# Optimization experiments

Hardware: AMD Instinct MI355X
Metric: run time of the kernel (lower is better)

The kernel has to match this reference:

```python
import jax, jax.numpy as jnp
import numpy as np


def make_hadamard(n, seed=1):
    # Sylvester Hadamard matrix with random sign diagonal, orthonormalized.
    assert (n & (n - 1)) == 0, 'n must be a power of 2'
    H = np.array([[1.0]], dtype=np.float32)
    while H.shape[0] < n:
        H = np.block([[H, H], [H, -H]])
    rng = np.random.default_rng(seed)
    signs = rng.choice(np.array([-1.0, 1.0], dtype=np.float32), size=n)
    H = (H * signs[None, :]) / np.sqrt(n, dtype=np.float32)
    return jnp.asarray(H)


def setup_inputs() -> dict:
    key = jax.random.key(0)
    k_x, = jax.random.split(key, 1)
    B, S, D = 4, 4096, 2048
    x = jax.random.normal(k_x, (B, S, D), dtype=jnp.float32)
    scale = jnp.ones((1,), dtype=jnp.float32) * 0.1  # must be > 0
    hadamard = make_hadamard(D)
    return {
        'x': x,
        'scale': scale,
        'hadamard': hadamard,
        'Qn': 8,
        'Qp': 7,
        'num_elements': B * S * D,
    }


def reference(x, scale, hadamard, Qn, Qp, num_elements):
    # grad_scale_mode == 'LSQ_grad_scale'
    qn = float(Qn)
    qp = float(Qp)
    grad_scale = 1.0 / jnp.sqrt(jnp.float32(num_elements) * qp)
    # scale = (scale - scale*gs).detach() + scale*gs  (forward value unchanged)
    bw_scale = scale * grad_scale
    s = jax.lax.stop_gradient(scale - bw_scale) + bw_scale  # shape [1]

    x_rot = jnp.matmul(x, hadamard)           # [B,S,D]
    xq = jnp.clip(x_rot / s, -qn, qp)
    # straight-through rounding: (round(x)-x).detach() + x
    yq = jax.lax.stop_gradient(jnp.round(xq) - xq) + xq
    y = yq * s
    return jnp.matmul(y, hadamard.T)          # un-rotate
```

## Files before the change

### kernel.cpp

```cpp
#include <hip/hip_runtime.h>
#include <math.h>


constexpr int D  = 2048;
constexpr int NR = 8;

__device__ __forceinline__ void fwht2048(float4 (&v)[NR], int lane) {
    #pragma unroll
    for (int r = 0; r < NR; ++r) {
        float a, b;
        a = v[r].x; b = v[r].y; v[r].x = a + b; v[r].y = a - b;
        a = v[r].z; b = v[r].w; v[r].z = a + b; v[r].w = a - b;
        a = v[r].x; b = v[r].z; v[r].x = a + b; v[r].z = a - b;
        a = v[r].y; b = v[r].w; v[r].y = a + b; v[r].w = a - b;
    }
    #pragma unroll
    for (int m = 1; m <= 32; m <<= 1) {
        const float sgn = (lane & m) ? -1.0f : 1.0f;
        #pragma unroll
        for (int r = 0; r < NR; ++r) {
            float ox = __shfl_xor(v[r].x, m, 64);
            float oy = __shfl_xor(v[r].y, m, 64);
            float oz = __shfl_xor(v[r].z, m, 64);
            float ow = __shfl_xor(v[r].w, m, 64);
            v[r].x = fmaf(sgn, v[r].x, ox);
            v[r].y = fmaf(sgn, v[r].y, oy);
            v[r].z = fmaf(sgn, v[r].z, oz);
            v[r].w = fmaf(sgn, v[r].w, ow);
        }
    }
    #pragma unroll
    for (int m = 1; m <= 4; m <<= 1) {
        #pragma unroll
        for (int r = 0; r < NR; ++r) {
            if ((r & m) == 0) {
                float4 a = v[r], b = v[r | m];
                v[r].x     = a.x + b.x; v[r].y     = a.y + b.y;
                v[r].z     = a.z + b.z; v[r].w     = a.w + b.w;
                v[r | m].x = a.x - b.x; v[r | m].y = a.y - b.y;
                v[r | m].z = a.z - b.z; v[r | m].w = a.w - b.w;
            }
        }
    }
}

__device__ __forceinline__ float quant1(float xh, float h0, float s, float inv_s,
                                        float nqn, float qp) {
    float t = xh * h0;
    float u = t * inv_s;
    u = fminf(fmaxf(u, nqn), qp);
    float q = rintf(u);
    return q * (s * h0);
}

__global__ __launch_bounds__(256) void lsq_fwht_kernel(
    const float* __restrict__ x,
    const float* __restrict__ scale,
    const float* __restrict__ hadamard,
    const int*   __restrict__ qn_p,
    const int*   __restrict__ qp_p,
    const int*   __restrict__ ne_p,
    float*       __restrict__ out,
    int rows)
{
    const int lane = threadIdx.x & 63;
    const int wave = threadIdx.x >> 6;
    const int row  = blockIdx.x * 4 + wave;
    if (row >= rows) return;

    const float sc    = scale[0];
    const float qp    = (float)qp_p[0];
    const float nqn   = -(float)qn_p[0];
    const float gs    = 1.0f / sqrtf((float)ne_p[0] * qp);
    const float bw    = sc * gs;
    const float s     = (sc - bw) + bw;
    const float inv_s = 1.0f / s;

    float4 v[NR], h[NR];
    {
        const float4* x4 = reinterpret_cast<const float4*>(x + (size_t)row * D) + lane;
        const float4* h4 = reinterpret_cast<const float4*>(hadamard) + lane;
        #pragma unroll
        for (int r = 0; r < NR; ++r) {
            v[r] = x4[(size_t)r * 64];
            h[r] = h4[(size_t)r * 64];
        }
    }

    fwht2048(v, lane);

    #pragma unroll
    for (int r = 0; r < NR; ++r) {
        v[r].x = quant1(v[r].x, h[r].x, s, inv_s, nqn, qp);
        v[r].y = quant1(v[r].y, h[r].y, s, inv_s, nqn, qp);
        v[r].z = quant1(v[r].z, h[r].z, s, inv_s, nqn, qp);
        v[r].w = quant1(v[r].w, h[r].w, s, inv_s, nqn, qp);
    }

    fwht2048(v, lane);

    {
        float4* y4 = reinterpret_cast<float4*>(out + (size_t)row * D) + lane;
        #pragma unroll
        for (int r = 0; r < NR; ++r) y4[(size_t)r * 64] = v[r];
    }
}

extern "C" void kernel_launch(void* const* d_in, const int* in_sizes, int n_in,
                              void* d_out, int out_size, void* d_ws, size_t ws_size,
                              hipStream_t stream) {
    const float* x        = (const float*)d_in[0];
    const float* scale    = (const float*)d_in[1];
    const float* hadamard = (const float*)d_in[2];
    const int*   Qn       = (const int*)d_in[3];
    const int*   Qp       = (const int*)d_in[4];
    const int*   ne       = (const int*)d_in[5];
    float*       out      = (float*)d_out;

    const int rows = in_sizes[0] / D;
    const int grid = (rows + 3) / 4;

    lsq_fwht_kernel<<<grid, 256, 0, stream>>>(x, scale, hadamard, Qn, Qp, ne,
                                              out, rows);
}
```

Measured before the change: 253.1 us.

## Replace cross-lane shuffle FWHT stages with swizzled LDS transposes

The 2048-point Walsh-Hadamard transform used to do its six cross-lane stages with 24 shuffles per element group. It now stages data through per-wave shared memory with XOR-swizzled layouts, so every butterfly runs on registers between two LDS transposes. The quantization step runs in the permuted layout, and the Hadamard sign row is loaded to match. This trades shuffle and ALU work for LDS traffic and waitcnt barriers. Correctness depends on the swizzle indexing lining up exactly, and wave-level ordering relies on plain lgkmcnt waits with no barrier.

```diff
diff --git a/kernel.cpp b/kernel.cpp
--- a/kernel.cpp
+++ b/kernel.cpp
@@ -5,7 +5,24 @@
 constexpr int D  = 2048;
 constexpr int NR = 8;
 
-__device__ __forceinline__ void fwht2048(float4 (&v)[NR], int lane) {
+#define LGKM0() __asm__ __volatile__("s_waitcnt lgkmcnt(0)" ::: "memory")
+
+__device__ __forceinline__ void bfly(float4& a, float4& b) {
+    float4 ta = a, tb = b;
+    a.x = ta.x + tb.x; a.y = ta.y + tb.y; a.z = ta.z + tb.z; a.w = ta.w + tb.w;
+    b.x = ta.x - tb.x; b.y = ta.y - tb.y; b.z = ta.z - tb.z; b.w = ta.w - tb.w;
+}
+
+__device__ __forceinline__ void reg_stages(float4 (&v)[NR]) {
+    #pragma unroll
+    for (int m = 1; m <= 4; m <<= 1) {
+        #pragma unroll
+        for (int r = 0; r < NR; ++r)
+            if ((r & m) == 0) bfly(v[r], v[r | m]);
+    }
+}
+
+__device__ __forceinline__ void comp_stages(float4 (&v)[NR]) {
     #pragma unroll
     for (int r = 0; r < NR; ++r) {
         float a, b;
@@ -14,40 +31,11 @@
         a = v[r].x; b = v[r].z; v[r].x = a + b; v[r].z = a - b;
         a = v[r].y; b = v[r].w; v[r].y = a + b; v[r].w = a - b;
     }
-    #pragma unroll
-    for (int m = 1; m <= 32; m <<= 1) {
-        const float sgn = (lane & m) ? -1.0f : 1.0f;
-        #pragma unroll
-        for (int r = 0; r < NR; ++r) {
-            float ox = __shfl_xor(v[r].x, m, 64);
-            float oy = __shfl_xor(v[r].y, m, 64);
-            float oz = __shfl_xor(v[r].z, m, 64);
-            float ow = __shfl_xor(v[r].w, m, 64);
-            v[r].x = fmaf(sgn, v[r].x, ox);
-            v[r].y = fmaf(sgn, v[r].y, oy);
-            v[r].z = fmaf(sgn, v[r].z, oz);
-            v[r].w = fmaf(sgn, v[r].w, ow);
-        }
-    }
-    #pragma unroll
-    for (int m = 1; m <= 4; m <<= 1) {
-        #pragma unroll
-        for (int r = 0; r < NR; ++r) {
-            if ((r & m) == 0) {
-                float4 a = v[r], b = v[r | m];
-                v[r].x     = a.x + b.x; v[r].y     = a.y + b.y;
-                v[r].z     = a.z + b.z; v[r].w     = a.w + b.w;
-                v[r | m].x = a.x - b.x; v[r | m].y = a.y - b.y;
-                v[r | m].z = a.z - b.z; v[r | m].w = a.w - b.w;
-            }
-        }
-    }
 }
 
 __device__ __forceinline__ float quant1(float xh, float h0, float s, float inv_s,
                                         float nqn, float qp) {
-    float t = xh * h0;
-    float u = t * inv_s;
+    float u = xh * h0 * inv_s;
     u = fminf(fmaxf(u, nqn), qp);
     float q = rintf(u);
     return q * (s * h0);
@@ -63,10 +51,16 @@
     float*       __restrict__ out,
     int rows)
 {
+    __shared__ float smem[4][D];
+
     const int lane = threadIdx.x & 63;
     const int wave = threadIdx.x >> 6;
     const int row  = blockIdx.x * 4 + wave;
     if (row >= rows) return;
+
+    float* lds = smem[wave];
+    const int llo = lane & 7;
+    const int lhi = lane >> 3;
 
     const float sc    = scale[0];
     const float qp    = (float)qp_p[0];
@@ -76,18 +70,41 @@
     const float s     = (sc - bw) + bw;
     const float inv_s = 1.0f / s;
 
-    float4 v[NR], h[NR];
+    float4 v[NR];
     {
         const float4* x4 = reinterpret_cast<const float4*>(x + (size_t)row * D) + lane;
-        const float4* h4 = reinterpret_cast<const float4*>(hadamard) + lane;
         #pragma unroll
-        for (int r = 0; r < NR; ++r) {
-            v[r] = x4[(size_t)r * 64];
-            h[r] = h4[(size_t)r * 64];
-        }
+        for (int r = 0; r < NR; ++r) v[r] = x4[(size_t)r * 64];
+    }
+    float4 h[NR];
+    {
+        const float4* h4 = reinterpret_cast<const float4*>(hadamard);
+        #pragma unroll
+        for (int r = 0; r < NR; ++r) h[r] = h4[lhi * 64 + r * 8 + llo];
     }
 
-    fwht2048(v, lane);
+    const int wA  = (lane * 4) ^ (lhi << 2);
+    const int rBb = lhi * 256 + llo * 32;
+    const int rCb = lhi * 256 + ((llo * 4) ^ (lhi << 2));
+
+    comp_stages(v);
+    reg_stages(v);
+    #pragma unroll
+    for (int r = 0; r < NR; ++r)
+        *reinterpret_cast<float4*>(lds + r * 256 + wA) = v[r];
+    LGKM0();
+    #pragma unroll
+    for (int r = 0; r < NR; ++r)
+        v[r] = *reinterpret_cast<const float4*>(lds + rBb + ((r * 4) ^ (llo << 2)));
+    reg_stages(v);
+    #pragma unroll
+    for (int r = 0; r < NR; ++r)
+        *reinterpret_cast<float4*>(lds + rBb + ((r * 4) ^ (lhi << 2))) = v[r];
+    LGKM0();
+    #pragma unroll
+    for (int r = 0; r < NR; ++r)
+        v[r] = *reinterpret_cast<const float4*>(lds + rCb + r * 32);
+    reg_stages(v);
 
     #pragma unroll
     for (int r = 0; r < NR; ++r) {
@@ -97,7 +114,24 @@
         v[r].w = quant1(v[r].w, h[r].w, s, inv_s, nqn, qp);
     }
 
-    fwht2048(v, lane);
+    reg_stages(v);
+    #pragma unroll
+    for (int r = 0; r < NR; ++r)
+        *reinterpret_cast<float4*>(lds + rCb + r * 32) = v[r];
+    LGKM0();
+    #pragma unroll
+    for (int r = 0; r < NR; ++r)
+        v[r] = *reinterpret_cast<const float4*>(lds + rBb + ((r * 4) ^ (lhi << 2)));
+    reg_stages(v);
+    #pragma unroll
+    for (int r = 0; r < NR; ++r)
+        *reinterpret_cast<float4*>(lds + rBb + ((r * 4) ^ (llo << 2))) = v[r];
+    LGKM0();
+    #pragma unroll
+    for (int r = 0; r < NR; ++r)
+        v[r] = *reinterpret_cast<const float4*>(lds + r * 256 + wA);
+    reg_stages(v);
+    comp_stages(v);
 
     {
         float4* y4 = reinterpret_cast<float4*>(out + (size_t)row * D) + lane;
```

Result: faster. 247.2 us (-2.3%).
